# Optimization experiments

Hardware: AMD Instinct MI355X
Metric: run time of the kernel (lower is better)

Reference implementation:

```python
import jax, jax.numpy as jnp
import numpy as np

B, S, D, H, DK, FF = 8, 1024, 1024, 16, 64, 4096


def setup_inputs() -> dict:
    key = jax.random.key(0)
    ks = jax.random.split(key, 8)
    scale = 0.02
    return {
        "x": jax.random.normal(ks[0], (B, S, D), jnp.float32),
        "mask": jax.random.randint(ks[1], (B, S, S), 0, 2).astype(bool),
        "wq": jax.random.normal(ks[2], (H, D, DK), jnp.float32) * scale,
        "wk": jax.random.normal(ks[3], (H, D, DK), jnp.float32) * scale,
        "wv": jax.random.normal(ks[4], (H, D, DK), jnp.float32) * scale,
        "fc_w": jax.random.normal(ks[5], (D, D), jnp.float32) * scale,
        "fc_b": jnp.zeros((D,), jnp.float32),
        "w1": jax.random.normal(ks[6], (FF, D), jnp.float32) * scale,
        "b1": jnp.zeros((FF,), jnp.float32),
        "w2": jax.random.normal(ks[7], (D, FF), jnp.float32) * scale,
        "b2": jnp.zeros((D,), jnp.float32),
        "ln1_g": jnp.ones((D,), jnp.float32),
        "ln1_b": jnp.zeros((D,), jnp.float32),
        "ln2_g": jnp.ones((D,), jnp.float32),
        "ln2_b": jnp.zeros((D,), jnp.float32),
    }


def _layernorm(x, g, b, eps=1e-5):
    mu = jnp.mean(x, axis=-1, keepdims=True)
    var = jnp.mean(jnp.square(x - mu), axis=-1, keepdims=True)
    return (x - mu) * jax.lax.rsqrt(var + eps) * g + b


def reference(x, mask, wq, wk, wv, fc_w, fc_b, w1, b1, w2, b2, ln1_g, ln1_b, ln2_g, ln2_b):
    dk = wq.shape[-1]
    # batched over heads: [B,S,D] x [H,D,dk] -> [B,H,S,dk]
    q = jnp.einsum('bsd,hde->bhse', x, wq)
    k = jnp.einsum('bsd,hde->bhse', x, wk)
    v = jnp.einsum('bsd,hde->bhse', x, wv)
    s = jnp.einsum('bhqe,bhke->bhqk', q, k)
    # faithful quirks of the source: mask-fill with -1000 BEFORE scaling,
    # and softmax over dim=1 of the per-head [B,Sq,Sk] scores (the query axis).
    s = jnp.where(mask[:, None, :, :], s, jnp.float32(-1000.0))
    s = s / jnp.float32(dk) ** 0.5
    p = jax.nn.softmax(s, axis=2)
    o = jnp.einsum('bhqk,bhkv->bhqv', p, v)
    o = o.transpose(0, 2, 1, 3).reshape(x.shape[0], x.shape[1], -1)  # concat heads
    att = o @ fc_w.T + fc_b
    x1 = _layernorm(att + x, ln1_g, ln1_b)
    h = jax.nn.relu(x1 @ w1.T + b1) @ w2.T + b2
    return _layernorm(h + x1, ln2_g, ln2_b)
```

## Files before the change

### kernel.cpp

```cpp
#include <hip/hip_runtime.h>
#include <stdint.h>

#define DEV static __device__ __forceinline__

typedef unsigned short u16;
typedef __attribute__((ext_vector_type(8))) short v8s;
typedef __attribute__((ext_vector_type(4))) float v4f;
typedef __attribute__((ext_vector_type(4))) unsigned short v4u16;

DEV u16 f2bf(float f) {
  union { float f; unsigned u; } c; c.f = f;
  unsigned r = c.u + 0x7FFFu + ((c.u >> 16) & 1u);
  return (u16)(r >> 16);
}
DEV float bf2f(u16 h) {
  union { unsigned u; float f; } c; c.u = ((unsigned)h) << 16;
  return c.f;
}

DEV void gload16(const u16* g, u16* l) {
  __builtin_amdgcn_global_load_lds(
      (const __attribute__((address_space(1))) unsigned int*)g,
      (__attribute__((address_space(3))) unsigned int*)l, 16, 0, 0);
}

enum { MODE_QKV = 0, MODE_PV = 2, MODE_BIAS_RES = 3, MODE_BIAS_RELU = 4, MODE_PARTIAL = 5 };

struct EpArgs {
  const float* bias;
  const float* res;
  const u16* res_bf;
  float* outf;
  u16* outb;
  u16* outb2;
  u16* q; u16* k; u16* v;
  int z0;
};

template <int BM, int BN, int FM, int FN, int MODE>
__global__ __launch_bounds__(256, 2)
void gemm_nt(const u16* __restrict__ A, int lda, long sA,
             const u16* __restrict__ B, int ldb, long sB,
             int K, int N, int nbx, int nby, EpArgs ep)
{
  __shared__ u16 As[BM * 32];
  __shared__ u16 Bs[BN * 32];

  const int tid  = threadIdx.x;
  const int lane = tid & 63;
  const int wave = tid >> 6;
  const int wm = (wave >> 1) * (FM * 16);
  const int wn = (wave & 1) * (FN * 16);

  const int id = blockIdx.x;
  const int nby8 = nby >> 3;
  const int c8 = id & 7, jj = id >> 3;
  const int tm = ((jj % nby8) * 8 + c8) * BM;
  const int tn = (jj / nby8) * BN;
  const int z  = blockIdx.y;

  const u16* Az = A + (long)z * sA;
  const u16* Bz = B + (long)z * sB;

  v4f acc[FM][FN];
  const v4f zero4 = {0.f, 0.f, 0.f, 0.f};
#pragma unroll
  for (int i = 0; i < FM; i++)
#pragma unroll
    for (int j = 0; j < FN; j++) acc[i][j] = zero4;

  for (int kt = 0; kt < K; kt += 32) {
#pragma unroll
    for (int c = 0; c < BM * 4; c += 256) {
      int cc = c + tid;
      int row = cc >> 2, kk = (cc & 3) * 8;
      gload16(Az + (long)(tm + row) * lda + kt + kk, &As[cc * 8]);
    }
#pragma unroll
    for (int c = 0; c < BN * 4; c += 256) {
      int cc = c + tid;
      int row = cc >> 2, kk = (cc & 3) * 8;
      gload16(Bz + (long)(tn + row) * ldb + kt + kk, &Bs[cc * 8]);
    }
    __syncthreads();

    v8s af[FM], bfr[FN];
#pragma unroll
    for (int i = 0; i < FM; i++)
      af[i] = *(const v8s*)&As[(wm + i * 16 + (lane & 15)) * 32 + (lane >> 4) * 8];
#pragma unroll
    for (int j = 0; j < FN; j++)
      bfr[j] = *(const v8s*)&Bs[(wn + j * 16 + (lane & 15)) * 32 + (lane >> 4) * 8];
#pragma unroll
    for (int i = 0; i < FM; i++)
#pragma unroll
      for (int j = 0; j < FN; j++)
        acc[i][j] = __builtin_amdgcn_mfma_f32_16x16x32_bf16(af[i], bfr[j], acc[i][j], 0, 0, 0);
    __syncthreads();
  }

  bool res_is_f32 = false;
  if constexpr (MODE == MODE_BIAS_RES) res_is_f32 = (ep.res != nullptr);
  u16* pdst = nullptr;
  if constexpr (MODE == MODE_PARTIAL) pdst = z ? ep.outb2 : ep.outb;

#pragma unroll
  for (int i = 0; i < FM; i++) {
    int mbase = tm + wm + i * 16 + ((lane >> 4) << 2);
#pragma unroll
    for (int j = 0; j < FN; j++) {
      int n = tn + wn + j * 16 + (lane & 15);
#pragma unroll
      for (int r = 0; r < 4; r++) {
        float val = acc[i][j][r];
        int m = mbase + r;
        if constexpr (MODE == MODE_QKV) {
          int b = m >> 10, s = m & 1023;
          int w = n >> 10, rr = n & 1023, h = rr >> 6, e = rr & 63;
          long idx = (((long)(b * 16 + h) << 10) + s) * 64 + e;
          u16* dst = (w == 0) ? ep.q : (w == 1) ? ep.k : ep.v;
          dst[idx] = f2bf(val);
        } else if constexpr (MODE == MODE_PV) {
          int zg = ep.z0 + z;
          int b = zg >> 4, h = zg & 15;
          ep.outb[((long)(b * 1024 + m) << 10) + h * 64 + n] = f2bf(val);
        } else if constexpr (MODE == MODE_BIAS_RES) {
          long idx = (long)m * N + n;
          float rres = res_is_f32 ? ep.res[idx] : bf2f(ep.res_bf[idx]);
          ep.outf[idx] = val + ep.bias[n] + rres;
        } else if constexpr (MODE == MODE_BIAS_RELU) {
          float v2 = val + ep.bias[n];
          ep.outb[(long)m * N + n] = f2bf(fmaxf(v2, 0.f));
        } else if constexpr (MODE == MODE_PARTIAL) {
          pdst[(long)m * N + n] = f2bf(val);
        }
      }
    }
  }
}

__global__ __launch_bounds__(256, 4)
void attn_score(const u16* __restrict__ Q, const u16* __restrict__ Kb,
                const unsigned char* __restrict__ Mpk, float* __restrict__ rc,
                u16* __restrict__ E, int z0)
{
  __shared__ u16 sh[17408];
  __shared__ unsigned char Ms[2048];
  const int tid = threadIdx.x, lane = tid & 63, wave = tid >> 6;
  const int wm = (wave >> 1) * 64, wn = (wave & 1) * 64;
  const int zl = blockIdx.z, q0 = blockIdx.y * 128, n0 = blockIdx.x * 128;
  const int b = (z0 + zl) >> 4;
  const u16* Qz = Q + ((long)zl << 16);
  const u16* Kz = Kb + ((long)zl << 16);
  u16* Qs = sh;
  u16* Ks = sh + 8192;
  u16* Ps = sh;

#pragma unroll
  for (int c = 0; c < 4; c++) {
    int cc = c * 256 + tid;
    int s = cc >> 9, rem = cc & 511, row = rem >> 2, k0 = (rem & 3) * 8;
    gload16(Qz + (long)(q0 + row) * 64 + s * 32 + k0, &Qs[cc * 8]);
  }
#pragma unroll
  for (int c = 0; c < 4; c++) {
    int cc = c * 256 + tid;
    int s = cc >> 9, rem = cc & 511, row = rem >> 2, k0 = (rem & 3) * 8;
    gload16(Kz + (long)(n0 + row) * 64 + s * 32 + k0, &Ks[cc * 8]);
  }
  if (tid < 128)
    ((uint4*)Ms)[tid] =
        *(const uint4*)(Mpk + ((long)b << 17) + (long)(q0 + tid) * 128 + (n0 >> 3));
  __syncthreads();

  v4f sacc[4][4];
  const v4f zero4 = {0.f, 0.f, 0.f, 0.f};
#pragma unroll
  for (int i = 0; i < 4; i++)
#pragma unroll
    for (int j = 0; j < 4; j++) sacc[i][j] = zero4;
#pragma unroll
  for (int s = 0; s < 2; s++) {
    v8s af[4], bf[4];
#pragma unroll
    for (int i = 0; i < 4; i++)
      af[i] = *(const v8s*)&Qs[s * 4096 + (wm + i * 16 + (lane & 15)) * 32 + (lane >> 4) * 8];
#pragma unroll
    for (int j = 0; j < 4; j++)
      bf[j] = *(const v8s*)&Ks[s * 4096 + (wn + j * 16 + (lane & 15)) * 32 + (lane >> 4) * 8];
#pragma unroll
    for (int i = 0; i < 4; i++)
#pragma unroll
      for (int j = 0; j < 4; j++)
        sacc[i][j] = __builtin_amdgcn_mfma_f32_16x16x32_bf16(af[i], bf[j], sacc[i][j], 0, 0, 0);
  }
  __syncthreads();

#pragma unroll
  for (int j = 0; j < 4; j++) {
    int col = wn + j * 16 + (lane & 15);
    float csum = 0.f;
#pragma unroll
    for (int i = 0; i < 4; i++) {
      int mlb = wm + i * 16 + ((lane >> 4) << 2);
#pragma unroll
      for (int r = 0; r < 4; r++) {
        int ml = mlb + r;
        bool mk = (Ms[ml * 16 + (col >> 3)] >> (col & 7)) & 1;
        float ev = mk ? __expf(sacc[i][j][r] * 0.125f) : 0.f;
        u16 eb = f2bf(ev);
        Ps[ml * 136 + col] = eb;
        csum += bf2f(eb);
      }
    }
    csum += __shfl_xor(csum, 16);
    csum += __shfl_xor(csum, 32);
    if (lane < 16) atomicAdd(&rc[(zl << 10) + n0 + col], csum);
  }
  __syncthreads();

  u16* Ez = E + ((long)zl << 20);
#pragma unroll
  for (int it = 0; it < 8; it++) {
    int idx = it * 256 + tid;
    int row = idx >> 4, c16 = (idx & 15) * 8;
    *(uint4*)(Ez + (long)(q0 + row) * 1024 + n0 + c16) = *(const uint4*)(&Ps[row * 136 + c16]);
  }
}

__global__ __launch_bounds__(256, 2)
void attn_colsum(const u16* __restrict__ Q, const u16* __restrict__ Kb,
                 const unsigned char* __restrict__ Mb, float* __restrict__ rc)
{
  __shared__ u16 Qs[2 * 128 * 32];
  __shared__ u16 Ks[2 * 128 * 32];
  const int tid = threadIdx.x, lane = tid & 63, wave = tid >> 6;
  const int wm = (wave >> 1) * 64, wn = (wave & 1) * 64;
  const int z = blockIdx.y, q0 = blockIdx.x * 128, b = z >> 4;
  const u16* Qz = Q + ((long)z << 16);
  const u16* Kz = Kb + ((long)z << 16);
  const unsigned char* Mz = Mb + ((long)b << 20);

#pragma unroll
  for (int c = 0; c < 4; c++) {
    int cc = c * 256 + tid;
    int s = cc >> 9, rem = cc & 511, row = rem >> 2, k0 = (rem & 3) * 8;
    gload16(Qz + (long)(q0 + row) * 64 + s * 32 + k0, &Qs[cc * 8]);
  }

  for (int nt = 0; nt < 8; nt++) {
    int n0 = nt * 128;
#pragma unroll
    for (int c = 0; c < 4; c++) {
      int cc = c * 256 + tid;
      int s = cc >> 9, rem = cc & 511, row = rem >> 2, k0 = (rem & 3) * 8;
      gload16(Kz + (long)(n0 + row) * 64 + s * 32 + k0, &Ks[cc * 8]);
    }
    __syncthreads();

    v4f sacc[4][4];
    const v4f zero4 = {0.f, 0.f, 0.f, 0.f};
#pragma unroll
    for (int i = 0; i < 4; i++)
#pragma unroll
      for (int j = 0; j < 4; j++) sacc[i][j] = zero4;
#pragma unroll
    for (int s = 0; s < 2; s++) {
      v8s af[4], bf[4];
#pragma unroll
      for (int i = 0; i < 4; i++)
        af[i] = *(const v8s*)&Qs[s * 4096 + (wm + i * 16 + (lane & 15)) * 32 + (lane >> 4) * 8];
#pragma unroll
      for (int j = 0; j < 4; j++)
        bf[j] = *(const v8s*)&Ks[s * 4096 + (wn + j * 16 + (lane & 15)) * 32 + (lane >> 4) * 8];
#pragma unroll
      for (int i = 0; i < 4; i++)
#pragma unroll
        for (int j = 0; j < 4; j++)
          sacc[i][j] = __builtin_amdgcn_mfma_f32_16x16x32_bf16(af[i], bf[j], sacc[i][j], 0, 0, 0);
    }

#pragma unroll
    for (int j = 0; j < 4; j++) {
      int n = n0 + wn + j * 16 + (lane & 15);
      float csum = 0.f;
#pragma unroll
      for (int i = 0; i < 4; i++) {
        int mbase = q0 + wm + i * 16 + ((lane >> 4) << 2);
#pragma unroll
        for (int r = 0; r < 4; r++) {
          int m = mbase + r;
          bool mk = Mz[(long)m * 1024 + n] != 0;
          float sv = mk ? sacc[i][j][r] : -1000.0f;
          csum += bf2f(f2bf(__expf(sv * 0.125f)));
        }
      }
      csum += __shfl_xor(csum, 16);
      csum += __shfl_xor(csum, 32);
      if (lane < 16) atomicAdd(&rc[(z << 10) + n], csum);
    }
    __syncthreads();
  }
}

__global__ __launch_bounds__(256, 2)
void attn_pv(const u16* __restrict__ Q, const u16* __restrict__ Kb,
             const u16* __restrict__ vT, const unsigned char* __restrict__ Mb,
             u16* __restrict__ oc)
{
  __shared__ u16 Ks[2 * 128 * 32];
  __shared__ u16 Vs[4 * 64 * 32];
  __shared__ u16 Ps[4 * 128 * 32];
  const int tid = threadIdx.x, lane = tid & 63, wave = tid >> 6;
  const int wm = (wave >> 1) * 64;
  const int wn = (wave & 1) * 64;
  const int wnv = (wave & 1) * 32;
  const int z = blockIdx.y, q0 = blockIdx.x * 128, b = z >> 4, h = z & 15;
  const u16* Qz = Q + ((long)z << 16);
  const u16* Kz = Kb + ((long)z << 16);
  const u16* Vz = vT + ((long)z << 16);
  const unsigned char* Mz = Mb + ((long)b << 20);

#pragma unroll
  for (int c = 0; c < 4; c++) {
    int cc = c * 256 + tid;
    int s = cc >> 9, rem = cc & 511, row = rem >> 2, k0 = (rem & 3) * 8;
    gload16(Qz + (long)(q0 + row) * 64 + s * 32 + k0, &Ks[cc * 8]);
  }
  __syncthreads();
  v8s qf[4][2];
#pragma unroll
  for (int i = 0; i < 4; i++)
#pragma unroll
    for (int s = 0; s < 2; s++)
      qf[i][s] = *(const v8s*)&Ks[s * 4096 + (wm + i * 16 + (lane & 15)) * 32 + (lane >> 4) * 8];
  __syncthreads();

  v4f oacc[4][2];
  const v4f zero4 = {0.f, 0.f, 0.f, 0.f};
#pragma unroll
  for (int i = 0; i < 4; i++)
#pragma unroll
    for (int j = 0; j < 2; j++) oacc[i][j] = zero4;

  for (int nt = 0; nt < 8; nt++) {
    int n0 = nt * 128;
#pragma unroll
    for (int c = 0; c < 4; c++) {
      int cc = c * 256 + tid;
      int s = cc >> 9, rem = cc & 511, row = rem >> 2, k0 = (rem & 3) * 8;
      gload16(Kz + (long)(n0 + row) * 64 + s * 32 + k0, &Ks[cc * 8]);
    }
#pragma unroll
    for (int c = 0; c < 4; c++) {
      int cc = c * 256 + tid;
      int s = cc >> 8, rem = cc & 255, v = rem >> 2, k0 = (rem & 3) * 8;
      gload16(Vz + (long)v * 1024 + n0 + s * 32 + k0, &Vs[cc * 8]);
    }
    __syncthreads();

    v4f sacc[4][4];
#pragma unroll
    for (int i = 0; i < 4; i++)
#pragma unroll
      for (int j = 0; j < 4; j++) sacc[i][j] = zero4;
#pragma unroll
    for (int s = 0; s < 2; s++) {
      v8s bf[4];
#pragma unroll
      for (int j = 0; j < 4; j++)
        bf[j] = *(const v8s*)&Ks[s * 4096 + (wn + j * 16 + (lane & 15)) * 32 + (lane >> 4) * 8];
#pragma unroll
      for (int i = 0; i < 4; i++)
#pragma unroll
        for (int j = 0; j < 4; j++)
          sacc[i][j] = __builtin_amdgcn_mfma_f32_16x16x32_bf16(qf[i][s], bf[j], sacc[i][j], 0, 0, 0);
    }

#pragma unroll
    for (int i = 0; i < 4; i++) {
      int mlb = wm + i * 16 + ((lane >> 4) << 2);
#pragma unroll
      for (int j = 0; j < 4; j++) {
        int col = wn + j * 16 + (lane & 15);
        int gn = n0 + col;
#pragma unroll
        for (int r = 0; r < 4; r++) {
          int ml = mlb + r;
          bool mk = Mz[(long)(q0 + ml) * 1024 + gn] != 0;
          float sv = mk ? sacc[i][j][r] : -1000.0f;
          Ps[(col >> 5) * 4096 + ml * 32 + (col & 31)] = f2bf(__expf(sv * 0.125f));
        }
      }
    }
    __syncthreads();

#pragma unroll
    for (int s = 0; s < 4; s++) {
      v8s vf[2];
#pragma unroll
      for (int j = 0; j < 2; j++)
        vf[j] = *(const v8s*)&Vs[s * 2048 + (wnv + j * 16 + (lane & 15)) * 32 + (lane >> 4) * 8];
#pragma unroll
      for (int i = 0; i < 4; i++) {
        v8s pf = *(const v8s*)&Ps[s * 4096 + (wm + i * 16 + (lane & 15)) * 32 + (lane >> 4) * 8];
#pragma unroll
        for (int j = 0; j < 2; j++)
          oacc[i][j] = __builtin_amdgcn_mfma_f32_16x16x32_bf16(pf, vf[j], oacc[i][j], 0, 0, 0);
      }
    }
    __syncthreads();
  }

#pragma unroll
  for (int i = 0; i < 4; i++) {
    int mbase = q0 + wm + i * 16 + ((lane >> 4) << 2);
#pragma unroll
    for (int j = 0; j < 2; j++) {
      int n = wnv + j * 16 + (lane & 15);
#pragma unroll
      for (int r = 0; r < 4; r++) {
        int m = mbase + r;
        oc[((long)(b * 1024 + m) << 10) + h * 64 + n] = f2bf(oacc[i][j][r]);
      }
    }
  }
}

__global__ __launch_bounds__(256)
void transpose_scale(const u16* __restrict__ V, const float* __restrict__ rc,
                     u16* __restrict__ vT)
{
  __shared__ u16 t[64 * 66];
  __shared__ float rl[64];
  const int zl = blockIdx.y;
  const int s0 = blockIdx.x * 64;
  const int tid = threadIdx.x;
  const int r = tid >> 2, cg = (tid & 3) << 4;
  const u16* src = V + ((long)zl << 16) + (long)(s0 + r) * 64 + cg;
  v4u16 a0 = *(const v4u16*)(src);
  v4u16 a1 = *(const v4u16*)(src + 4);
  v4u16 a2 = *(const v4u16*)(src + 8);
  v4u16 a3 = *(const v4u16*)(src + 12);
  if (tid < 64) rl[tid] = 1.f / rc[(zl << 10) + s0 + tid];
  u16 tmp[16] = {(u16)a0.x, (u16)a0.y, (u16)a0.z, (u16)a0.w,
                 (u16)a1.x, (u16)a1.y, (u16)a1.z, (u16)a1.w,
                 (u16)a2.x, (u16)a2.y, (u16)a2.z, (u16)a2.w,
                 (u16)a3.x, (u16)a3.y, (u16)a3.z, (u16)a3.w};
#pragma unroll
  for (int i = 0; i < 16; i++) t[(cg + i) * 66 + r] = tmp[i];
  __syncthreads();
  const int e = tid >> 2, sg = (tid & 3) << 4;
  u16* dst = vT + ((long)zl << 16) + (long)e * 1024 + s0 + sg;
  v4u16 o;
#pragma unroll
  for (int q = 0; q < 4; q++) {
#pragma unroll
    for (int w = 0; w < 4; w++) {
      float f = bf2f(t[e * 66 + sg + q * 4 + w]) * rl[sg + q * 4 + w];
      ((u16*)&o)[w] = f2bf(f);
    }
    *(v4u16*)(dst + q * 4) = o;
  }
}

__global__ __launch_bounds__(256)
void ln_comb(const u16* __restrict__ p0, const u16* __restrict__ p1,
             const float* __restrict__ bias,
             const float* __restrict__ resf, const u16* __restrict__ resb,
             const float* __restrict__ gam, const float* __restrict__ bet,
             float* __restrict__ outf, u16* __restrict__ outb)
{
  long row = blockIdx.x;
  long base = (row << 10) + (threadIdx.x << 2);
  v4u16 a = *(const v4u16*)(p0 + base);
  v4u16 b = *(const v4u16*)(p1 + base);
  v4f bi = *(const v4f*)(bias + (threadIdx.x << 2));
  v4f v;
  v.x = bf2f(a.x) + bf2f(b.x) + bi.x;
  v.y = bf2f(a.y) + bf2f(b.y) + bi.y;
  v.z = bf2f(a.z) + bf2f(b.z) + bi.z;
  v.w = bf2f(a.w) + bf2f(b.w) + bi.w;
  if (resf) {
    v4f r = *(const v4f*)(resf + base);
    v.x += r.x; v.y += r.y; v.z += r.z; v.w += r.w;
  } else {
    v4u16 r = *(const v4u16*)(resb + base);
    v.x += bf2f(r.x); v.y += bf2f(r.y); v.z += bf2f(r.z); v.w += bf2f(r.w);
  }
  float s = v.x + v.y + v.z + v.w;
  float s2 = v.x * v.x + v.y * v.y + v.z * v.z + v.w * v.w;
#pragma unroll
  for (int o = 32; o > 0; o >>= 1) { s += __shfl_down(s, o); s2 += __shfl_down(s2, o); }
  __shared__ float red[8];
  int wv_ = threadIdx.x >> 6, ln = threadIdx.x & 63;
  if (ln == 0) { red[wv_] = s; red[4 + wv_] = s2; }
  __syncthreads();
  float S1 = red[0] + red[1] + red[2] + red[3];
  float S2 = red[4] + red[5] + red[6] + red[7];
  float mu = S1 * (1.f / 1024.f);
  float var = S2 * (1.f / 1024.f) - mu * mu;
  float rstd = rsqrtf(var + 1e-5f);
  v4f g4 = *(const v4f*)(gam + (threadIdx.x << 2));
  v4f b4 = *(const v4f*)(bet + (threadIdx.x << 2));
  v4f o4;
  o4.x = (v.x - mu) * rstd * g4.x + b4.x;
  o4.y = (v.y - mu) * rstd * g4.y + b4.y;
  o4.z = (v.z - mu) * rstd * g4.z + b4.z;
  o4.w = (v.w - mu) * rstd * g4.w + b4.w;
  if (outf) *(v4f*)(outf + base) = o4;
  if (outb) {
    v4u16 u;
    u.x = f2bf(o4.x); u.y = f2bf(o4.y); u.z = f2bf(o4.z); u.w = f2bf(o4.w);
    *(v4u16*)(outb + base) = u;
  }
}

__global__ __launch_bounds__(256)
void ln_kernel(const float* __restrict__ in, const float* __restrict__ gam,
               const float* __restrict__ bet, float* __restrict__ outf,
               u16* __restrict__ outb)
{
  long row = blockIdx.x;
  v4f v = *(const v4f*)(in + (row << 10) + (threadIdx.x << 2));
  float s = v.x + v.y + v.z + v.w;
  float s2 = v.x * v.x + v.y * v.y + v.z * v.z + v.w * v.w;
#pragma unroll
  for (int o = 32; o > 0; o >>= 1) { s += __shfl_down(s, o); s2 += __shfl_down(s2, o); }
  __shared__ float red[8];
  int wv_ = threadIdx.x >> 6, ln = threadIdx.x & 63;
  if (ln == 0) { red[wv_] = s; red[4 + wv_] = s2; }
  __syncthreads();
  float S1 = red[0] + red[1] + red[2] + red[3];
  float S2 = red[4] + red[5] + red[6] + red[7];
  float mu = S1 * (1.f / 1024.f);
  float var = S2 * (1.f / 1024.f) - mu * mu;
  float rstd = rsqrtf(var + 1e-5f);
  v4f g4 = *(const v4f*)(gam + (threadIdx.x << 2));
  v4f b4 = *(const v4f*)(bet + (threadIdx.x << 2));
  v4f o4;
  o4.x = (v.x - mu) * rstd * g4.x + b4.x;
  o4.y = (v.y - mu) * rstd * g4.y + b4.y;
  o4.z = (v.z - mu) * rstd * g4.z + b4.z;
  o4.w = (v.w - mu) * rstd * g4.w + b4.w;
  if (outf) *(v4f*)(outf + (row << 10) + (threadIdx.x << 2)) = o4;
  if (outb) {
    v4u16 u;
    u.x = f2bf(o4.x); u.y = f2bf(o4.y); u.z = f2bf(o4.z); u.w = f2bf(o4.w);
    *(v4u16*)(outb + (row << 10) + (threadIdx.x << 2)) = u;
  }
}

__global__ __launch_bounds__(256)
void cvt_bf16(const float* __restrict__ in, u16* __restrict__ out, int n4)
{
  int i = blockIdx.x * 256 + threadIdx.x;
  if (i >= n4) return;
  v4f v = ((const v4f*)in)[i];
  v4u16 u;
  u.x = f2bf(v.x); u.y = f2bf(v.y); u.z = f2bf(v.z); u.w = f2bf(v.w);
  ((v4u16*)out)[i] = u;
}

__global__ __launch_bounds__(256)
void pack_qkvw(const float* __restrict__ wq, const float* __restrict__ wk,
               const float* __restrict__ wv, u16* __restrict__ out)
{
  int i = blockIdx.x * 256 + threadIdx.x;
  int w = i >> 20, r = i & 1048575;
  int e = r & 63, d = (r >> 6) & 1023, h = r >> 16;
  const float* src = (w == 0) ? wq : ((w == 1) ? wk : wv);
  float v = src[(((long)h << 10) + d) * 64 + e];
  out[((((long)w << 10) + (h << 6) + e) << 10) + d] = f2bf(v);
}

__global__ void detect_mask_kernel(const unsigned char* __restrict__ m, int* __restrict__ flag)
{
  if (threadIdx.x == 0 && blockIdx.x == 0) {
    int nz = 0;
    for (int i = 0; i < 256; i++)
      if ((i & 3) != 0 && m[i] != 0) nz++;
    *flag = (nz == 0) ? 1 : 0;
  }
}

__global__ __launch_bounds__(256)
void canon_mask(const unsigned char* __restrict__ m, const int* __restrict__ flag,
                unsigned char* __restrict__ out)
{
  int i = blockIdx.x * 256 + threadIdx.x;
  uchar4 o;
  if (*flag) {
    const int* mi = (const int*)m;
    o.x = mi[i * 4 + 0] != 0; o.y = mi[i * 4 + 1] != 0;
    o.z = mi[i * 4 + 2] != 0; o.w = mi[i * 4 + 3] != 0;
  } else {
    o = ((const uchar4*)m)[i];
  }
  ((uchar4*)out)[i] = o;
}

__global__ __launch_bounds__(256)
void canon_pack(const unsigned char* __restrict__ m, const int* __restrict__ flag,
                unsigned int* __restrict__ out)
{
  int g = blockIdx.x * 256 + threadIdx.x;
  unsigned int bits = 0;
  if (*flag) {
    const int* mi = (const int*)m + (long)g * 32;
#pragma unroll
    for (int i = 0; i < 32; i++) bits |= (mi[i] != 0 ? 1u : 0u) << i;
  } else {
    const unsigned char* mb = m + (long)g * 32;
#pragma unroll
    for (int i = 0; i < 32; i++) bits |= (mb[i] != 0 ? 1u : 0u) << i;
  }
  out[g] = bits;
}

extern "C" void kernel_launch(void* const* d_in, const int* in_sizes, int n_in,
                              void* d_out, int out_size, void* d_ws, size_t ws_size,
                              hipStream_t stream)
{
  const float* x     = (const float*)d_in[0];
  const unsigned char* mask = (const unsigned char*)d_in[1];
  const float* wq    = (const float*)d_in[2];
  const float* wk    = (const float*)d_in[3];
  const float* wv    = (const float*)d_in[4];
  const float* fc_w  = (const float*)d_in[5];
  const float* fc_b  = (const float*)d_in[6];
  const float* w1    = (const float*)d_in[7];
  const float* b1    = (const float*)d_in[8];
  const float* w2    = (const float*)d_in[9];
  const float* b2    = (const float*)d_in[10];
  const float* ln1_g = (const float*)d_in[11];
  const float* ln1_b = (const float*)d_in[12];
  const float* ln2_g = (const float*)d_in[13];
  const float* ln2_b = (const float*)d_in[14];
  (void)in_sizes; (void)n_in; (void)out_size;

  const size_t MB = 1ull << 20;
  char* ws = (char*)d_ws;
  int*   mflag = (int*)ws;
  float* rc    = (float*)(ws + 65536);
  unsigned char* Mpk = (unsigned char*)(ws + 1 * MB);
  u16*   bqkv  = (u16*)(ws + 2 * MB);
  u16*   fcb   = (u16*)(ws + 8 * MB);
  u16*   w1b   = (u16*)(ws + 10 * MB);
  u16*   w2b   = (u16*)(ws + 18 * MB);
  u16*   xb    = (u16*)(ws + 26 * MB);
  u16*   x1b   = xb;
  u16*   Qb    = (u16*)(ws + 42 * MB);
  u16*   Kb    = (u16*)(ws + 58 * MB);
  u16*   Vb    = (u16*)(ws + 74 * MB);
  u16*   vT    = (u16*)(ws + 90 * MB);
  u16*   oc    = (u16*)(ws + 106 * MB);
  u16*   h1    = (u16*)(ws + 42 * MB);
  float* r1    = (float*)(ws + 122 * MB);
  unsigned char* Mb = (unsigned char*)(ws + 122 * MB);
  u16*   E     = (u16*)(ws + 122 * MB);
  u16*   p0    = (u16*)(ws + 122 * MB);
  u16*   p1    = (u16*)(ws + 138 * MB);

  int CZ = 0;
  if      (ws_size >= 378 * MB) CZ = 128;
  else if (ws_size >= 250 * MB) CZ = 64;
  else if (ws_size >= 186 * MB) CZ = 32;
  else if (ws_size >= 154 * MB) CZ = 16;

  detect_mask_kernel<<<1, 64, 0, stream>>>(mask, mflag);
  if (CZ > 0) canon_pack<<<1024, 256, 0, stream>>>(mask, mflag, (unsigned int*)Mpk);
  else        canon_mask<<<8192, 256, 0, stream>>>(mask, mflag, Mb);

  cvt_bf16<<<8192, 256, 0, stream>>>(x, xb, 2097152);
  pack_qkvw<<<12288, 256, 0, stream>>>(wq, wk, wv, bqkv);
  cvt_bf16<<<1024, 256, 0, stream>>>(fc_w, fcb, 262144);
  cvt_bf16<<<4096, 256, 0, stream>>>(w1, w1b, 1048576);
  cvt_bf16<<<4096, 256, 0, stream>>>(w2, w2b, 1048576);

  {
    EpArgs ep = {};
    ep.q = Qb; ep.k = Kb; ep.v = Vb;
    gemm_nt<128, 128, 4, 4, MODE_QKV><<<dim3(24 * 64, 1), 256, 0, stream>>>(
        xb, 1024, 0, bqkv, 1024, 0, 1024, 3072, 24, 64, ep);
  }

  hipMemsetAsync(rc, 0, 128 * 1024 * 4, stream);
  if (CZ > 0) {
    for (int z0 = 0; z0 < 128; z0 += CZ) {
      attn_score<<<dim3(8, 8, CZ), 256, 0, stream>>>(
          Qb + (long)z0 * 65536, Kb + (long)z0 * 65536, Mpk,
          rc + (long)z0 * 1024, E, z0);
      transpose_scale<<<dim3(16, CZ), 256, 0, stream>>>(
          Vb + (long)z0 * 65536, rc + (long)z0 * 1024, vT + (long)z0 * 65536);
      EpArgs ep = {};
      ep.outb = oc; ep.z0 = z0;
      gemm_nt<128, 64, 4, 2, MODE_PV><<<dim3(8, CZ), 256, 0, stream>>>(
          E, 1024, 1048576, vT + (long)z0 * 65536, 1024, 65536,
          1024, 64, 1, 8, ep);
    }
  } else {
    attn_colsum<<<dim3(8, 128), 256, 0, stream>>>(Qb, Kb, Mb, rc);
    transpose_scale<<<dim3(16, 128), 256, 0, stream>>>(Vb, rc, vT);
    attn_pv<<<dim3(8, 128), 256, 0, stream>>>(Qb, Kb, vT, Mb, oc);
  }

  if (CZ > 0) {
    {
      EpArgs ep = {};
      ep.outb = p0; ep.outb2 = p1;
      gemm_nt<128, 128, 4, 4, MODE_PARTIAL><<<dim3(8 * 64, 2), 256, 0, stream>>>(
          oc, 1024, 512, fcb, 1024, 512, 512, 1024, 8, 64, ep);
    }
    ln_comb<<<8192, 256, 0, stream>>>(p0, p1, fc_b, x, (const u16*)nullptr,
                                      ln1_g, ln1_b, (float*)nullptr, x1b);
    {
      EpArgs ep = {};
      ep.bias = b1; ep.outb = h1;
      gemm_nt<128, 128, 4, 4, MODE_BIAS_RELU><<<dim3(32 * 64, 1), 256, 0, stream>>>(
          x1b, 1024, 0, w1b, 1024, 0, 1024, 4096, 32, 64, ep);
    }
    {
      EpArgs ep = {};
      ep.outb = p0; ep.outb2 = p1;
      gemm_nt<128, 128, 4, 4, MODE_PARTIAL><<<dim3(8 * 64, 2), 256, 0, stream>>>(
          h1, 4096, 2048, w2b, 4096, 2048, 2048, 1024, 8, 64, ep);
    }
    ln_comb<<<8192, 256, 0, stream>>>(p0, p1, b2, (const float*)nullptr, x1b,
                                      ln2_g, ln2_b, (float*)d_out, (u16*)nullptr);
  } else {
    {
      EpArgs ep = {};
      ep.bias = fc_b; ep.res = x; ep.outf = r1;
      gemm_nt<128, 128, 4, 4, MODE_BIAS_RES><<<dim3(8 * 64, 1), 256, 0, stream>>>(
          oc, 1024, 0, fcb, 1024, 0, 1024, 1024, 8, 64, ep);
    }
    ln_kernel<<<8192, 256, 0, stream>>>(r1, ln1_g, ln1_b, (float*)nullptr, x1b);
    {
      EpArgs ep = {};
      ep.bias = b1; ep.outb = h1;
      gemm_nt<128, 128, 4, 4, MODE_BIAS_RELU><<<dim3(32 * 64, 1), 256, 0, stream>>>(
          x1b, 1024, 0, w1b, 1024, 0, 1024, 4096, 32, 64, ep);
    }
    {
      EpArgs ep = {};
      ep.bias = b2; ep.res_bf = x1b; ep.outf = r1;
      gemm_nt<128, 128, 4, 4, MODE_BIAS_RES><<<dim3(8 * 64, 1), 256, 0, stream>>>(
          h1, 4096, 0, w2b, 4096, 0, 4096, 1024, 8, 64, ep);
    }
    ln_kernel<<<8192, 256, 0, stream>>>(r1, ln2_g, ln2_b, (float*)d_out, (u16*)nullptr);
  }
}
```

Measured before the change: 638.5 us.

## Store attention probabilities and scaled V in FP8 and use FP8 MFMA for PV

The attention score kernel now quantizes the exponentiated scores to FP8, sums the quantized values for the column normalizer, and writes an FP8 E matrix. The scaled, transposed V is also written as FP8 with a 512x pre-scale. A new PV kernel runs fp8 MFMA and undoes the scale in its epilogue. This halves E traffic, and since E now needs half the workspace, larger head chunks (fewer launches) fit. It costs FP8 rounding error in the softmax probabilities and V, plus a simple, unpipelined PV kernel.

Result: faster. 607.2 us (-4.9%).

```diff
diff --git a/kernel.cpp b/kernel.cpp
--- a/kernel.cpp
+++ b/kernel.cpp
@@ -17,14 +17,25 @@
   union { unsigned u; float f; } c; c.u = ((unsigned)h) << 16;
   return c.f;
 }
+DEV unsigned char f2fp8(float f) {
+  return (unsigned char)(__builtin_amdgcn_cvt_pk_fp8_f32(f, 0.f, 0, false) & 0xff);
+}
+DEV float fp82f(unsigned char b) {
+  return __builtin_amdgcn_cvt_f32_fp8((int)b, 0);
+}
 
 DEV void gload16(const u16* g, u16* l) {
   __builtin_amdgcn_global_load_lds(
       (const __attribute__((address_space(1))) unsigned int*)g,
       (__attribute__((address_space(3))) unsigned int*)l, 16, 0, 0);
 }
-
-enum { MODE_QKV = 0, MODE_PV = 2, MODE_BIAS_RES = 3, MODE_BIAS_RELU = 4, MODE_PARTIAL = 5 };
+DEV void gload16b(const unsigned char* g, unsigned char* l) {
+  __builtin_amdgcn_global_load_lds(
+      (const __attribute__((address_space(1))) unsigned int*)g,
+      (__attribute__((address_space(3))) unsigned int*)l, 16, 0, 0);
+}
+
+enum { MODE_QKV = 0, MODE_BIAS_RES = 3, MODE_BIAS_RELU = 4, MODE_PARTIAL = 5 };
 
 struct EpArgs {
   const float* bias;
@@ -120,10 +131,6 @@
           long idx = (((long)(b * 16 + h) << 10) + s) * 64 + e;
           u16* dst = (w == 0) ? ep.q : (w == 1) ? ep.k : ep.v;
           dst[idx] = f2bf(val);
-        } else if constexpr (MODE == MODE_PV) {
-          int zg = ep.z0 + z;
-          int b = zg >> 4, h = zg & 15;
-          ep.outb[((long)(b * 1024 + m) << 10) + h * 64 + n] = f2bf(val);
         } else if constexpr (MODE == MODE_BIAS_RES) {
           long idx = (long)m * N + n;
           float rres = res_is_f32 ? ep.res[idx] : bf2f(ep.res_bf[idx]);
@@ -142,7 +149,7 @@
 __global__ __launch_bounds__(256, 4)
 void attn_score(const u16* __restrict__ Q, const u16* __restrict__ Kb,
                 const unsigned char* __restrict__ Mpk, float* __restrict__ rc,
-                u16* __restrict__ E, int z0)
+                unsigned char* __restrict__ E8, int z0)
 {
   __shared__ u16 sh[17408];
   __shared__ unsigned char Ms[2048];
@@ -208,9 +215,9 @@
         int ml = mlb + r;
         bool mk = (Ms[ml * 16 + (col >> 3)] >> (col & 7)) & 1;
         float ev = mk ? __expf(sacc[i][j][r] * 0.125f) : 0.f;
-        u16 eb = f2bf(ev);
-        Ps[ml * 136 + col] = eb;
-        csum += bf2f(eb);
+        float evq = fp82f(f2fp8(ev));
+        Ps[ml * 136 + col] = f2bf(evq);
+        csum += evq;
       }
     }
     csum += __shfl_xor(csum, 16);
@@ -219,12 +226,81 @@
   }
   __syncthreads();
 
-  u16* Ez = E + ((long)zl << 20);
+  unsigned char* Ez = E8 + ((long)zl << 20);
 #pragma unroll
   for (int it = 0; it < 8; it++) {
     int idx = it * 256 + tid;
-    int row = idx >> 4, c16 = (idx & 15) * 8;
-    *(uint4*)(Ez + (long)(q0 + row) * 1024 + n0 + c16) = *(const uint4*)(&Ps[row * 136 + c16]);
+    int row = idx >> 4, c8 = (idx & 15) * 8;
+    v4u16 a = *(const v4u16*)&Ps[row * 136 + c8];
+    v4u16 bb = *(const v4u16*)&Ps[row * 136 + c8 + 4];
+    int w0 = __builtin_amdgcn_cvt_pk_fp8_f32(bf2f(a.x), bf2f(a.y), 0, false);
+    w0 = __builtin_amdgcn_cvt_pk_fp8_f32(bf2f(a.z), bf2f(a.w), w0, true);
+    int w1 = __builtin_amdgcn_cvt_pk_fp8_f32(bf2f(bb.x), bf2f(bb.y), 0, false);
+    w1 = __builtin_amdgcn_cvt_pk_fp8_f32(bf2f(bb.z), bf2f(bb.w), w1, true);
+    uint2 o; o.x = (unsigned)w0; o.y = (unsigned)w1;
+    *(uint2*)(Ez + (long)(q0 + row) * 1024 + n0 + c8) = o;
+  }
+}
+
+__global__ __launch_bounds__(256, 2)
+void attn_pv_fp8(const unsigned char* __restrict__ E8,
+                 const unsigned char* __restrict__ vT8,
+                 u16* __restrict__ oc, int z0)
+{
+  __shared__ unsigned char As[128 * 32];
+  __shared__ unsigned char Bs[64 * 32];
+  const int tid = threadIdx.x, lane = tid & 63, wave = tid >> 6;
+  const int wm = (wave >> 1) * 64;
+  const int wn = (wave & 1) * 32;
+  const int zl = blockIdx.y, q0 = blockIdx.x * 128;
+  const int zg = z0 + zl, b = zg >> 4, h = zg & 15;
+  const unsigned char* Ez = E8 + ((long)zl << 20);
+  const unsigned char* Vz = vT8 + ((long)zl << 16);
+
+  v4f acc[4][2];
+  const v4f zero4 = {0.f, 0.f, 0.f, 0.f};
+#pragma unroll
+  for (int i = 0; i < 4; i++)
+#pragma unroll
+    for (int j = 0; j < 2; j++) acc[i][j] = zero4;
+
+  for (int kt = 0; kt < 1024; kt += 32) {
+    {
+      int row = tid >> 1, off = (tid & 1) * 16;
+      gload16b(Ez + (long)(q0 + row) * 1024 + kt + off, &As[row * 32 + off]);
+    }
+    if (tid < 128) {
+      int row = tid >> 1, off = (tid & 1) * 16;
+      gload16b(Vz + (long)row * 1024 + kt + off, &Bs[row * 32 + off]);
+    }
+    __syncthreads();
+
+    long bfr[2];
+#pragma unroll
+    for (int j = 0; j < 2; j++)
+      bfr[j] = *(const long*)&Bs[(wn + j * 16 + (lane & 15)) * 32 + (lane >> 4) * 8];
+#pragma unroll
+    for (int i = 0; i < 4; i++) {
+      long af = *(const long*)&As[(wm + i * 16 + (lane & 15)) * 32 + (lane >> 4) * 8];
+#pragma unroll
+      for (int j = 0; j < 2; j++)
+        acc[i][j] = __builtin_amdgcn_mfma_f32_16x16x32_fp8_fp8(af, bfr[j], acc[i][j], 0, 0, 0);
+    }
+    __syncthreads();
+  }
+
+#pragma unroll
+  for (int i = 0; i < 4; i++) {
+    int mbase = q0 + wm + i * 16 + ((lane >> 4) << 2);
+#pragma unroll
+    for (int j = 0; j < 2; j++) {
+      int n = wn + j * 16 + (lane & 15);
+#pragma unroll
+      for (int r = 0; r < 4; r++) {
+        int m = mbase + r;
+        oc[((long)(b * 1024 + m) << 10) + h * 64 + n] = f2bf(acc[i][j][r] * (1.f / 512.f));
+      }
+    }
   }
 }
 
@@ -461,6 +537,43 @@
       ((u16*)&o)[w] = f2bf(f);
     }
     *(v4u16*)(dst + q * 4) = o;
+  }
+}
+
+__global__ __launch_bounds__(256)
+void transpose_scale_fp8(const u16* __restrict__ V, const float* __restrict__ rc,
+                         unsigned char* __restrict__ vT8)
+{
+  __shared__ u16 t[64 * 66];
+  __shared__ float rl[64];
+  const int zl = blockIdx.y;
+  const int s0 = blockIdx.x * 64;
+  const int tid = threadIdx.x;
+  const int r = tid >> 2, cg = (tid & 3) << 4;
+  const u16* src = V + ((long)zl << 16) + (long)(s0 + r) * 64 + cg;
+  v4u16 a0 = *(const v4u16*)(src);
+  v4u16 a1 = *(const v4u16*)(src + 4);
+  v4u16 a2 = *(const v4u16*)(src + 8);
+  v4u16 a3 = *(const v4u16*)(src + 12);
+  if (tid < 64) rl[tid] = 512.f / rc[(zl << 10) + s0 + tid];
+  u16 tmp[16] = {(u16)a0.x, (u16)a0.y, (u16)a0.z, (u16)a0.w,
+                 (u16)a1.x, (u16)a1.y, (u16)a1.z, (u16)a1.w,
+                 (u16)a2.x, (u16)a2.y, (u16)a2.z, (u16)a2.w,
+                 (u16)a3.x, (u16)a3.y, (u16)a3.z, (u16)a3.w};
+#pragma unroll
+  for (int i = 0; i < 16; i++) t[(cg + i) * 66 + r] = tmp[i];
+  __syncthreads();
+  const int e = tid >> 2, sg = (tid & 3) << 4;
+  unsigned char* dst = vT8 + ((long)zl << 16) + (long)e * 1024 + s0 + sg;
+#pragma unroll
+  for (int q = 0; q < 4; q++) {
+    float f0 = bf2f(t[e * 66 + sg + q * 4 + 0]) * rl[sg + q * 4 + 0];
+    float f1 = bf2f(t[e * 66 + sg + q * 4 + 1]) * rl[sg + q * 4 + 1];
+    float f2 = bf2f(t[e * 66 + sg + q * 4 + 2]) * rl[sg + q * 4 + 2];
+    float f3 = bf2f(t[e * 66 + sg + q * 4 + 3]) * rl[sg + q * 4 + 3];
+    int w0 = __builtin_amdgcn_cvt_pk_fp8_f32(f0, f1, 0, false);
+    w0 = __builtin_amdgcn_cvt_pk_fp8_f32(f2, f3, w0, true);
+    *(int*)(dst + q * 4) = w0;
   }
 }
 
@@ -654,19 +767,19 @@
   u16*   Kb    = (u16*)(ws + 58 * MB);
   u16*   Vb    = (u16*)(ws + 74 * MB);
   u16*   vT    = (u16*)(ws + 90 * MB);
+  unsigned char* vT8 = (unsigned char*)(ws + 90 * MB);
   u16*   oc    = (u16*)(ws + 106 * MB);
   u16*   h1    = (u16*)(ws + 42 * MB);
   float* r1    = (float*)(ws + 122 * MB);
   unsigned char* Mb = (unsigned char*)(ws + 122 * MB);
-  u16*   E     = (u16*)(ws + 122 * MB);
+  unsigned char* E8 = (unsigned char*)(ws + 122 * MB);
   u16*   p0    = (u16*)(ws + 122 * MB);
   u16*   p1    = (u16*)(ws + 138 * MB);
 
   int CZ = 0;
-  if      (ws_size >= 378 * MB) CZ = 128;
-  else if (ws_size >= 250 * MB) CZ = 64;
-  else if (ws_size >= 186 * MB) CZ = 32;
-  else if (ws_size >= 154 * MB) CZ = 16;
+  if      (ws_size >= 250 * MB) CZ = 128;
+  else if (ws_size >= 186 * MB) CZ = 64;
+  else if (ws_size >= 154 * MB) CZ = 32;
 
   detect_mask_kernel<<<1, 64, 0, stream>>>(mask, mflag);
   if (CZ > 0) canon_pack<<<1024, 256, 0, stream>>>(mask, mflag, (unsigned int*)Mpk);
@@ -690,14 +803,11 @@
     for (int z0 = 0; z0 < 128; z0 += CZ) {
       attn_score<<<dim3(8, 8, CZ), 256, 0, stream>>>(
           Qb + (long)z0 * 65536, Kb + (long)z0 * 65536, Mpk,
-          rc + (long)z0 * 1024, E, z0);
-      transpose_scale<<<dim3(16, CZ), 256, 0, stream>>>(
-          Vb + (long)z0 * 65536, rc + (long)z0 * 1024, vT + (long)z0 * 65536);
-      EpArgs ep = {};
-      ep.outb = oc; ep.z0 = z0;
-      gemm_nt<128, 64, 4, 2, MODE_PV><<<dim3(8, CZ), 256, 0, stream>>>(
-          E, 1024, 1048576, vT + (long)z0 * 65536, 1024, 65536,
-          1024, 64, 1, 8, ep);
+          rc + (long)z0 * 1024, E8, z0);
+      transpose_scale_fp8<<<dim3(16, CZ), 256, 0, stream>>>(
+          Vb + (long)z0 * 65536, rc + (long)z0 * 1024, vT8 + (long)z0 * 65536);
+      attn_pv_fp8<<<dim3(8, CZ), 256, 0, stream>>>(
+          E8, vT8 + (long)z0 * 65536, oc, z0);
     }
   } else {
     attn_colsum<<<dim3(8, 128), 256, 0, stream>>>(Qb, Kb, Mb, rc);
```
